# Kernel optimization log

Hardware: AMD Instinct MI355X
Metric: run time of the kernel (lower is better)

The kernel has to match this reference:

```python
import jax, jax.numpy as jnp
import numpy as np

B, T, H = 4, 2048, 1024
NH = 16
HD = H // NH  # 64
FF = 4 * H


def setup_inputs() -> dict:
    key = jax.random.key(0)
    ks = jax.random.split(key, 11)
    s = 0.02
    return {
        "x": jax.random.normal(ks[0], (B, T, H), dtype=jnp.float32),
        "Wq": jax.random.normal(ks[1], (H, H), dtype=jnp.float32) * s,
        "bq": jnp.zeros((H,), dtype=jnp.float32),
        "Wk": jax.random.normal(ks[2], (H, H), dtype=jnp.float32) * s,
        "bk": jnp.zeros((H,), dtype=jnp.float32),
        "Wv": jax.random.normal(ks[3], (H, H), dtype=jnp.float32) * s,
        "bv": jnp.zeros((H,), dtype=jnp.float32),
        "W1": jax.random.normal(ks[4], (H, FF), dtype=jnp.float32) * s,
        "b1": jnp.zeros((FF,), dtype=jnp.float32),
        "W2": jax.random.normal(ks[5], (FF, H), dtype=jnp.float32) * s,
        "b2": jnp.zeros((H,), dtype=jnp.float32),
    }


def _block(x, Wq, bq, Wk, bk, Wv, bv, W1, b1, W2, b2):
    b, t, h = x.shape
    # multi-head masked self-attention; NOTE: scale = full h_dim ** 0.5 (as in source)
    q = (x @ Wq + bq).reshape(b, t, NH, HD).transpose(0, 2, 1, 3)  # [B,nH,T,HD]
    k = (x @ Wk + bk).reshape(b, t, NH, HD).transpose(0, 2, 1, 3)
    v = (x @ Wv + bv).reshape(b, t, NH, HD).transpose(0, 2, 1, 3)
    att = jnp.einsum("bnqd,bnkd->bnqk", q, k) / (h ** 0.5)  # [B,nH,T,T]
    causal = jnp.tril(jnp.ones((t, t), dtype=bool))
    att = jnp.where(causal, att, -jnp.inf)
    w = jax.nn.softmax(att, axis=-1)
    attn_out = jnp.einsum("bnqk,bnkd->bnqd", w, v).transpose(0, 2, 1, 3).reshape(b, t, h)
    x = x + attn_out
    # MLP (dropout p=0 -> identity)
    mlp = jax.nn.gelu(x @ W1 + b1) @ W2 + b2
    return x + mlp


def reference(x, Wq, bq, Wk, bk, Wv, bv, W1, b1, W2, b2):
    return _block(x, Wq, bq, Wk, bk, Wv, bv, W1, b1, W2, b2)
```

## Files before the change

### kernel.cpp

```cpp
#include <hip/hip_runtime.h>
#include <cstdint>
#include <cstddef>

typedef unsigned short u16;
typedef __attribute__((ext_vector_type(8))) __bf16 bf16x8;
typedef __attribute__((ext_vector_type(4))) __bf16 bf16x4;
typedef __attribute__((ext_vector_type(4))) float f32x4;
typedef __attribute__((ext_vector_type(4))) u16 u16x4;

#define MFMA(a, b, c) __builtin_amdgcn_mfma_f32_16x16x32_bf16((a), (b), (c), 0, 0, 0)

__device__ __forceinline__ u16 f2b(float f) {
  union { __bf16 h; u16 u; } v;
  v.h = (__bf16)f;
  return v.u;
}

__device__ __forceinline__ void gld16(const void* g, void* l) {
  __builtin_amdgcn_global_load_lds(
      (__attribute__((address_space(1))) void*)(void*)(g),
      (__attribute__((address_space(3))) void*)(l), 16, 0, 0);
}

__device__ __forceinline__ size_t qk_off(int t, int hd) {
  return (size_t)((((t >> 4) * 2 + (hd >> 5)) * 512)
                  + ((((hd >> 3) & 3) * 16 + (t & 15)) * 8) + (hd & 7));
}
__device__ __forceinline__ size_t v_off(int t, int hd) {
  int kk = ((t & 15) << 2) | ((t >> 4) & 3);
  return (size_t)(((t >> 6) * 4096)
                  + (((hd >> 4) * 2 + (kk >> 5)) * 512)
                  + ((((kk >> 3) & 3) * 16 + (hd & 15)) * 8) + (kk & 7));
}

__global__ void xconv(const float* __restrict__ in, u16* __restrict__ out, int n) {
  int i = (blockIdx.x * blockDim.x + threadIdx.x) * 4;
  if (i >= n) return;
  float4 v = *(const float4*)(in + i);
  u16x4 o;
  o[0] = f2b(v.x); o[1] = f2b(v.y); o[2] = f2b(v.z); o[3] = f2b(v.w);
  *(u16x4*)(out + i) = o;
}

__global__ void wtrans_all(const float* __restrict__ Wq, const float* __restrict__ Wk,
                           const float* __restrict__ Wv, const float* __restrict__ W1,
                           const float* __restrict__ W2, u16* __restrict__ Wqkvt,
                           u16* __restrict__ W1t, u16* __restrict__ W2t) {
  __shared__ float tile[32][33];
  int blk = blockIdx.x;
  const float* W;
  u16* Wt;
  int Kd, Nd, nx;
  if (blk < 3072) {
    int s = blk >> 10;
    blk &= 1023;
    W = (s == 0) ? Wq : (s == 1) ? Wk : Wv;
    Wt = Wqkvt + (size_t)s * 1048576;
    Kd = 1024; Nd = 1024; nx = 32;
  } else if (blk < 7168) {
    blk -= 3072; W = W1; Wt = W1t; Kd = 1024; Nd = 4096; nx = 128;
  } else {
    blk -= 7168; W = W2; Wt = W2t; Kd = 4096; Nd = 1024; nx = 32;
  }
  int n0 = (blk % nx) * 32, k0 = (blk / nx) * 32;
  int tx = threadIdx.x, ty = threadIdx.y;
#pragma unroll
  for (int i = 0; i < 4; i++)
    tile[ty + i * 8][tx] = W[(size_t)(k0 + ty + i * 8) * Nd + n0 + tx];
  __syncthreads();
#pragma unroll
  for (int i = 0; i < 4; i++)
    Wt[(size_t)(n0 + ty + i * 8) * Kd + k0 + tx] = f2b(tile[tx][ty + i * 8]);
}

template <int MODE>
__global__ __launch_bounds__(512, 2) void gemm8p(
    const u16* __restrict__ A, const u16* __restrict__ Bt,
    const float* __restrict__ b0, void* __restrict__ outp,
    int N, int K) {
  __shared__ __attribute__((aligned(16))) u16 As_[2][16384];
  __shared__ __attribute__((aligned(16))) u16 Bs_[2][16384];
  const int tid = threadIdx.x;
  const int wid = tid >> 6, lane = tid & 63;
  const int g = lane >> 4, r = lane & 15;

  const int xcd = blockIdx.x & 7;
  const int ii = blockIdx.x >> 3;
  const int c4 = ii >> 4, w = ii & 15;
  const int bm = xcd * 4 + (w >> 2);
  const int bn = c4 * 4 + (w & 3);

  const int mrow = (wid >> 2) * 64;
  const int ncol = (wid & 3) * 32;

  const int ko0 = ((0 * 4 + g) ^ (r & 7)) * 8;
  const int ko1 = ((1 * 4 + g) ^ (r & 7)) * 8;

  size_t aOff[4], bOff[4];
#pragma unroll
  for (int i4 = 0; i4 < 4; i4++) {
    int cc = i4 * 512 + tid, row = cc >> 3;
    int js = ((cc & 7) ^ (row & 7)) * 8;
    aOff[i4] = (size_t)(bm * 256 + row) * K + js;
    bOff[i4] = (size_t)(bn * 256 + row) * K + js;
  }

  f32x4 acc[8][4];
  const f32x4 zero4 = {0.f, 0.f, 0.f, 0.f};
#pragma unroll
  for (int i = 0; i < 8; i++)
#pragma unroll
    for (int j = 0; j < 4; j++) acc[i][j] = zero4;

#pragma unroll
  for (int i4 = 0; i4 < 4; i4++) {
    gld16(A + aOff[i4], &As_[0][(i4 * 512 + tid) * 8]);
    gld16(Bt + bOff[i4], &Bs_[0][(i4 * 512 + tid) * 8]);
  }
  gld16(A + aOff[0] + 64, &As_[1][(0 * 512 + tid) * 8]);
  gld16(A + aOff[1] + 64, &As_[1][(1 * 512 + tid) * 8]);
  gld16(Bt + bOff[2] + 64, &Bs_[1][(2 * 512 + tid) * 8]);
  gld16(Bt + bOff[3] + 64, &Bs_[1][(3 * 512 + tid) * 8]);
  asm volatile("s_waitcnt vmcnt(4)" ::: "memory");
  __builtin_amdgcn_s_barrier();

  const int KT = K >> 6;
  for (int t = 0; t < KT; ++t) {
    const int p = t & 1, pn = p ^ 1;
    const u16* as = As_[p];
    const u16* bs = Bs_[p];
    const bool m1 = (t + 1) < KT, m2 = (t + 2) < KT;
    const size_t k1 = (size_t)(t + 1) * 64, k2 = (size_t)(t + 2) * 64;
    bf16x8 af[4][2], bf[2][2];

#pragma unroll
    for (int mt = 0; mt < 4; mt++) {
      int rw = mrow + mt * 16 + r;
      af[mt][0] = *(const bf16x8*)&as[rw * 64 + ko0];
      af[mt][1] = *(const bf16x8*)&as[rw * 64 + ko1];
    }
#pragma unroll
    for (int nt = 0; nt < 2; nt++) {
      int rw = ncol + nt * 16 + r;
      bf[nt][0] = *(const bf16x8*)&bs[rw * 64 + ko0];
      bf[nt][1] = *(const bf16x8*)&bs[rw * 64 + ko1];
    }
    if (m1) {
      gld16(A + aOff[2] + k1, &As_[pn][(1024 + tid) * 8]);
      gld16(A + aOff[3] + k1, &As_[pn][(1536 + tid) * 8]);
    }
    __builtin_amdgcn_s_barrier();
    asm volatile("s_waitcnt lgkmcnt(0)" ::: "memory");
    __builtin_amdgcn_sched_barrier(0);
    __builtin_amdgcn_s_setprio(1);
#pragma unroll
    for (int mt = 0; mt < 4; mt++)
#pragma unroll
      for (int nt = 0; nt < 2; nt++)
        acc[mt][nt] = MFMA(af[mt][1], bf[nt][1], MFMA(af[mt][0], bf[nt][0], acc[mt][nt]));
    __builtin_amdgcn_s_setprio(0);
    __builtin_amdgcn_s_barrier();

#pragma unroll
    for (int nt = 0; nt < 2; nt++) {
      int rw = 128 + ncol + nt * 16 + r;
      bf[nt][0] = *(const bf16x8*)&bs[rw * 64 + ko0];
      bf[nt][1] = *(const bf16x8*)&bs[rw * 64 + ko1];
    }
    if (m1) {
      gld16(Bt + bOff[0] + k1, &Bs_[pn][(tid) * 8]);
      gld16(Bt + bOff[1] + k1, &Bs_[pn][(512 + tid) * 8]);
    }
    __builtin_amdgcn_s_barrier();
    asm volatile("s_waitcnt lgkmcnt(0)" ::: "memory");
    __builtin_amdgcn_sched_barrier(0);
    __builtin_amdgcn_s_setprio(1);
#pragma unroll
    for (int mt = 0; mt < 4; mt++)
#pragma unroll
      for (int nt = 0; nt < 2; nt++)
        acc[mt][2 + nt] = MFMA(af[mt][1], bf[nt][1], MFMA(af[mt][0], bf[nt][0], acc[mt][2 + nt]));
    __builtin_amdgcn_s_setprio(0);
    __builtin_amdgcn_s_barrier();

#pragma unroll
    for (int mt = 0; mt < 4; mt++) {
      int rw = 128 + mrow + mt * 16 + r;
      af[mt][0] = *(const bf16x8*)&as[rw * 64 + ko0];
      af[mt][1] = *(const bf16x8*)&as[rw * 64 + ko1];
    }
    if (m2) {
      gld16(A + aOff[0] + k2, &As_[p][(tid) * 8]);
      gld16(A + aOff[1] + k2, &As_[p][(512 + tid) * 8]);
    }
    __builtin_amdgcn_s_barrier();
    asm volatile("s_waitcnt lgkmcnt(0)" ::: "memory");
    __builtin_amdgcn_sched_barrier(0);
    __builtin_amdgcn_s_setprio(1);
#pragma unroll
    for (int mt = 0; mt < 4; mt++)
#pragma unroll
      for (int nt = 0; nt < 2; nt++)
        acc[4 + mt][2 + nt] = MFMA(af[mt][1], bf[nt][1], MFMA(af[mt][0], bf[nt][0], acc[4 + mt][2 + nt]));
    __builtin_amdgcn_s_setprio(0);
    __builtin_amdgcn_s_barrier();

#pragma unroll
    for (int nt = 0; nt < 2; nt++) {
      int rw = ncol + nt * 16 + r;
      bf[nt][0] = *(const bf16x8*)&bs[rw * 64 + ko0];
      bf[nt][1] = *(const bf16x8*)&bs[rw * 64 + ko1];
    }
    if (m2) {
      gld16(Bt + bOff[2] + k2, &Bs_[p][(1024 + tid) * 8]);
      gld16(Bt + bOff[3] + k2, &Bs_[p][(1536 + tid) * 8]);
    }
    __builtin_amdgcn_s_barrier();
    asm volatile("s_waitcnt lgkmcnt(0)" ::: "memory");
    __builtin_amdgcn_sched_barrier(0);
    __builtin_amdgcn_s_setprio(1);
#pragma unroll
    for (int mt = 0; mt < 4; mt++)
#pragma unroll
      for (int nt = 0; nt < 2; nt++)
        acc[4 + mt][nt] = MFMA(af[mt][1], bf[nt][1], MFMA(af[mt][0], bf[nt][0], acc[4 + mt][nt]));
    __builtin_amdgcn_s_setprio(0);
    if (m2) asm volatile("s_waitcnt vmcnt(4)" ::: "memory");
    else    asm volatile("s_waitcnt vmcnt(0)" ::: "memory");
    __builtin_amdgcn_s_barrier();
  }

#pragma unroll
  for (int am = 0; am < 8; am++) {
#pragma unroll
    for (int an = 0; an < 4; an++) {
      int col = bn * 256 + (an >> 1) * 128 + ncol + (an & 1) * 16 + r;
      float bv = b0[col];
#pragma unroll
      for (int q = 0; q < 4; q++) {
        int row = bm * 256 + (am >> 2) * 128 + mrow + (am & 3) * 16 + g * 4 + q;
        float v = acc[am][an][q] + bv;
        if (MODE == 2) {
          const float c1 = -2.3025850929940457f;
          const float c2 = c1 * 0.044715f;
          float t2 = v * v;
          float z = v * (c1 + c2 * t2);
          float sg = 1.0f / (1.0f + __builtin_amdgcn_exp2f(z));
          ((u16*)outp)[(size_t)row * N + col] = f2b(v * sg);
        }
      }
    }
  }
}

template <int MODE>
__global__ __launch_bounds__(512, 2) void gemm256(
    const u16* __restrict__ A, const u16* __restrict__ Bt,
    const float* __restrict__ b0, const float* __restrict__ b1,
    const float* __restrict__ b2, void* __restrict__ outp,
    const float* __restrict__ resid, int N, int K, float scale) {
  __shared__ __attribute__((aligned(16))) u16 As_[3][16384];
  __shared__ __attribute__((aligned(16))) u16 Bs_[3][8192];
  const int tid = threadIdx.x;
  const int wid = tid >> 6, lane = tid & 63;
  const int g = lane >> 4, r = lane & 15;

  const int xcd = blockIdx.x & 7;
  const int ii = blockIdx.x >> 3;
  const int bm = xcd * 4 + ((ii & 31) >> 3);
  const int bn = (ii >> 5) * 8 + (ii & 7);

  const int wrow = (wid >> 1) * 64;
  const int wcol = (wid & 1) * 64;

  const int ko0 = ((0 * 4 + g) ^ (r & 7)) * 8;
  const int ko1 = ((1 * 4 + g) ^ (r & 7)) * 8;

  size_t aOff[4], bOff[2];
#pragma unroll
  for (int i4 = 0; i4 < 4; i4++) {
    int cc = i4 * 512 + tid, row = cc >> 3;
    int js = ((cc & 7) ^ (row & 7)) * 8;
    aOff[i4] = (size_t)(bm * 256 + row) * K + js;
  }
#pragma unroll
  for (int i2 = 0; i2 < 2; i2++) {
    int cc = i2 * 512 + tid, row = cc >> 3;
    int js = ((cc & 7) ^ (row & 7)) * 8;
    bOff[i2] = (size_t)(bn * 128 + row) * K + js;
  }

  f32x4 acc[4][4];
  const f32x4 zero4 = {0.f, 0.f, 0.f, 0.f};
#pragma unroll
  for (int i = 0; i < 4; i++)
#pragma unroll
    for (int j = 0; j < 4; j++) acc[i][j] = zero4;

#pragma unroll
  for (int i4 = 0; i4 < 4; i4++) gld16(A + aOff[i4], &As_[0][(i4 * 512 + tid) * 8]);
#pragma unroll
  for (int i2 = 0; i2 < 2; i2++) gld16(Bt + bOff[i2], &Bs_[0][(i2 * 512 + tid) * 8]);
#pragma unroll
  for (int i4 = 0; i4 < 4; i4++) gld16(A + aOff[i4] + 64, &As_[1][(i4 * 512 + tid) * 8]);
#pragma unroll
  for (int i2 = 0; i2 < 2; i2++) gld16(Bt + bOff[i2] + 64, &Bs_[1][(i2 * 512 + tid) * 8]);
  asm volatile("s_waitcnt vmcnt(6)" ::: "memory");
  __builtin_amdgcn_s_barrier();

  const int KT = K >> 6;
  int cur = 0;
  for (int t = 0; t < KT; ++t) {
    const u16* as = As_[cur];
    const u16* bs = Bs_[cur];
    const int stg = (cur == 0) ? 2 : cur - 1;
    const bool more = (t + 2) < KT;
    const size_t k2 = (size_t)(t + 2) * 64;

    bf16x8 af0[4], bf0[4], af1[4], bf1[4];
#pragma unroll
    for (int mt = 0; mt < 4; mt++) {
      af0[mt] = *(const bf16x8*)&as[(wrow + mt * 16 + r) * 64 + ko0];
      af1[mt] = *(const bf16x8*)&as[(wrow + mt * 16 + r) * 64 + ko1];
    }
#pragma unroll
    for (int nt = 0; nt < 4; nt++) {
      bf0[nt] = *(const bf16x8*)&bs[(wcol + nt * 16 + r) * 64 + ko0];
      bf1[nt] = *(const bf16x8*)&bs[(wcol + nt * 16 + r) * 64 + ko1];
    }

    if (more) {
#pragma unroll
      for (int i4 = 0; i4 < 4; i4++)
        gld16(A + aOff[i4] + k2, &As_[stg][(i4 * 512 + tid) * 8]);
#pragma unroll
      for (int i2 = 0; i2 < 2; i2++)
        gld16(Bt + bOff[i2] + k2, &Bs_[stg][(i2 * 512 + tid) * 8]);
    }

#pragma unroll
    for (int mt = 0; mt < 4; mt++)
#pragma unroll
      for (int nt = 0; nt < 4; nt++)
        acc[mt][nt] = MFMA(af0[mt], bf0[nt], acc[mt][nt]);
#pragma unroll
    for (int mt = 0; mt < 4; mt++)
#pragma unroll
      for (int nt = 0; nt < 4; nt++)
        acc[mt][nt] = MFMA(af1[mt], bf1[nt], acc[mt][nt]);

    if (t + 1 < KT) {
      if (more) asm volatile("s_waitcnt vmcnt(6)" ::: "memory");
      else      asm volatile("s_waitcnt vmcnt(0)" ::: "memory");
    }
    __builtin_amdgcn_s_barrier();
    cur = (cur == 2) ? 0 : cur + 1;
  }

#pragma unroll
  for (int mt = 0; mt < 4; mt++) {
#pragma unroll
    for (int nt = 0; nt < 4; nt++) {
      int col = bn * 128 + wcol + nt * 16 + r;
      float bv;
      if (MODE == 4) {
        int sec = col >> 10, hcol = col & 1023;
        bv = (sec == 0) ? b0[hcol] : (sec == 1) ? b1[hcol] : b2[hcol];
      } else {
        bv = b0[col];
      }
#pragma unroll
      for (int q = 0; q < 4; q++) {
        int row = bm * 256 + wrow + mt * 16 + g * 4 + q;
        float v = acc[mt][nt][q] + bv;
        if (MODE == 3) {
          ((float*)outp)[(size_t)row * N + col] = v + resid[(size_t)row * N + col];
        } else if (MODE == 4) {
          int sec = col >> 10, hcol = col & 1023;
          int head = hcol >> 6, hd = hcol & 63;
          int bb = row >> 11, tt = row & 2047;
          size_t hbase = ((size_t)bb * 16 + head) * 131072;
          u16* qout = (u16*)outp;
          if (sec == 0) {
            qout[hbase + qk_off(tt, hd)] = f2b(v * scale);
          } else if (sec == 1) {
            (qout + 8388608)[hbase + qk_off(tt, hd)] = f2b(v);
          } else {
            (qout + 16777216)[hbase + v_off(tt, hd)] = f2b(v);
          }
        }
      }
    }
  }
}

__global__ __launch_bounds__(256) void attn_kernel(
    const u16* __restrict__ Q, const u16* __restrict__ Kc,
    const u16* __restrict__ Vt, const float* __restrict__ x,
    float* __restrict__ x1, u16* __restrict__ xb1) {
  const int bh = blockIdx.x & 63;
  const int slot = blockIdx.x >> 6;
  const int tid = threadIdx.x;
  const int wid = tid >> 6, lane = tid & 63;
  const int g = lane >> 4, c = lane & 15;
  const u16* Qh = Q + (size_t)bh * 131072;
  const u16* Kh = Kc + (size_t)bh * 131072;
  const u16* Vh = Vt + (size_t)bh * 131072;
  const int b = bh >> 4, head = bh & 15;

  __shared__ __attribute__((aligned(16))) u16 Ks[8192];
  __shared__ __attribute__((aligned(16))) u16 Vs[8192];
  __shared__ __attribute__((aligned(16))) u16 P[4][32][72];

  bf16x8 ones;
#pragma unroll
  for (int i = 0; i < 8; i++) ones[i] = (__bf16)1.0f;

  const f32x4 zero4 = {0.f, 0.f, 0.f, 0.f};

  for (int phase = 0; phase < 2; ++phase) {
    const int bt = phase ? (15 - slot) : slot;
    const int q0b = bt * 128;
    const int q0 = q0b + wid * 32;
    const int kendw = q0 + 32;
    const int nkt = bt + 1;

    bf16x8 qf[2][2];
#pragma unroll
    for (int mt = 0; mt < 2; mt++)
#pragma unroll
      for (int h = 0; h < 2; h++)
        qf[mt][h] = *(const bf16x8*)&Qh[(((q0 >> 4) + mt) * 2 + h) * 512 + lane * 8];

    f32x4 o[2][4];
    f32x4 lac[2];
#pragma unroll
    for (int mt = 0; mt < 2; mt++) {
      lac[mt] = zero4;
#pragma unroll
      for (int i = 0; i < 4; i++) o[mt][i] = zero4;
    }

    for (int kt = 0; kt < nkt; ++kt) {
      const int k0 = kt * 128;
#pragma unroll
      for (int r2 = 0; r2 < 4; r2++) {
        int idx = (r2 * 256 + tid) * 8;
        gld16(Kh + (size_t)k0 * 64 + idx, Ks + idx);
        gld16(Vh + (size_t)k0 * 64 + idx, Vs + idx);
      }
      __syncthreads();

#pragma unroll
      for (int s2 = 0; s2 < 2; ++s2) {
        const int k0s = k0 + s2 * 64;
        if (k0s < kendw) {
          bf16x8 kf[4][2], vf[4][2];
#pragma unroll
          for (int nt = 0; nt < 4; nt++)
#pragma unroll
            for (int h = 0; h < 2; h++) {
              kf[nt][h] = *(const bf16x8*)&Ks[s2 * 4096 + (nt * 2 + h) * 512 + lane * 8];
              vf[nt][h] = *(const bf16x8*)&Vs[s2 * 4096 + (nt * 2 + h) * 512 + lane * 8];
            }

          f32x4 sv[2][4];
#pragma unroll
          for (int mt = 0; mt < 2; mt++)
#pragma unroll
            for (int nt = 0; nt < 4; nt++) sv[mt][nt] = zero4;
#pragma unroll
          for (int nt = 0; nt < 4; nt++)
#pragma unroll
            for (int mt = 0; mt < 2; mt++) {
              sv[mt][nt] = MFMA(qf[mt][0], kf[nt][0], sv[mt][nt]);
              sv[mt][nt] = MFMA(qf[mt][1], kf[nt][1], sv[mt][nt]);
            }

          if (k0s + 64 > q0) {
#pragma unroll
            for (int mt = 0; mt < 2; mt++)
#pragma unroll
              for (int rr = 0; rr < 4; rr++) {
                int q = q0 + mt * 16 + g * 4 + rr;
#pragma unroll
                for (int nt = 0; nt < 4; nt++)
                  if (k0s + nt * 16 + c > q) sv[mt][nt][rr] = -1e30f;
              }
          }

#pragma unroll
          for (int mt = 0; mt < 2; mt++)
#pragma unroll
            for (int rr = 0; rr < 4; rr++) {
              union { u16x4 u; bf16x4 h; } pw;
#pragma unroll
              for (int nt = 0; nt < 4; nt++)
                pw.h[nt] = (__bf16)__builtin_amdgcn_exp2f(sv[mt][nt][rr]);
              *(u16x4*)&P[wid][mt * 16 + g * 4 + rr][4 * c] = pw.u;
            }

          asm volatile("s_waitcnt lgkmcnt(0)" ::: "memory");

#pragma unroll
          for (int mt = 0; mt < 2; mt++) {
            bf16x8 pf0 = *(const bf16x8*)&P[wid][mt * 16 + c][g * 8];
            bf16x8 pf1 = *(const bf16x8*)&P[wid][mt * 16 + c][32 + g * 8];
            lac[mt] = MFMA(pf0, ones, lac[mt]);
            lac[mt] = MFMA(pf1, ones, lac[mt]);
#pragma unroll
            for (int ot = 0; ot < 4; ot++) {
              f32x4 oo = MFMA(pf0, vf[ot][0], o[mt][ot]);
              o[mt][ot] = MFMA(pf1, vf[ot][1], oo);
            }
          }
        }
      }
      __syncthreads();
    }

    float inv[2][4];
#pragma unroll
    for (int mt = 0; mt < 2; mt++)
#pragma unroll
      for (int rr = 0; rr < 4; rr++) inv[mt][rr] = 1.0f / lac[mt][rr];
#pragma unroll
    for (int mt = 0; mt < 2; mt++)
#pragma unroll
      for (int ot = 0; ot < 4; ot++)
#pragma unroll
        for (int rr = 0; rr < 4; rr++) {
          int t = q0 + mt * 16 + g * 4 + rr;
          int hd = ot * 16 + c;
          size_t xi = ((size_t)b * 2048 + t) * 1024 + head * 64 + hd;
          float v = x[xi] + o[mt][ot][rr] * inv[mt][rr];
          x1[xi] = v;
          xb1[xi] = f2b(v);
        }
  }
}

extern "C" void kernel_launch(void* const* d_in, const int* in_sizes, int n_in,
                              void* d_out, int out_size, void* d_ws, size_t ws_size,
                              hipStream_t stream) {
  (void)in_sizes; (void)n_in; (void)out_size; (void)ws_size;
  const float* x = (const float*)d_in[0];
  const float* Wq = (const float*)d_in[1];
  const float* bq = (const float*)d_in[2];
  const float* Wk = (const float*)d_in[3];
  const float* bk = (const float*)d_in[4];
  const float* Wv = (const float*)d_in[5];
  const float* bv = (const float*)d_in[6];
  const float* W1 = (const float*)d_in[7];
  const float* b1 = (const float*)d_in[8];
  const float* W2 = (const float*)d_in[9];
  const float* b2 = (const float*)d_in[10];

  char* ws = (char*)d_ws;
  size_t off = 0;
  auto alloc = [&](size_t bytes) {
    char* p = ws + off;
    off += (bytes + 255) & ~(size_t)255;
    return p;
  };
  u16* xb    = (u16*)alloc(8192ull * 1024 * 2);
  u16* Wqkvt = (u16*)alloc(3072ull * 1024 * 2);
  u16* W1t   = (u16*)alloc(4096ull * 1024 * 2);
  u16* W2t   = (u16*)alloc(1024ull * 4096 * 2);
  u16* Qb    = (u16*)alloc(3ull * 8192 * 1024 * 2);
  float* x1  = (float*)alloc(8192ull * 1024 * 4);
  u16* hb    = (u16*)alloc(8192ull * 4096 * 2);
  u16* xb1   = xb;
  u16* Kb    = Qb + 8388608;
  u16* Vtb   = Qb + 16777216;

  const float qscale = 1.4426950408889634f / 32.0f;

  xconv<<<dim3(8192), dim3(256), 0, stream>>>(x, xb, 8192 * 1024);
  wtrans_all<<<dim3(11264), dim3(32, 8), 0, stream>>>(
      Wq, Wk, Wv, W1, W2, Wqkvt, W1t, W2t);
  gemm256<4><<<dim3(768), dim3(512), 0, stream>>>(
      xb, Wqkvt, bq, bk, bv, Qb, nullptr, 3072, 1024, qscale);
  attn_kernel<<<dim3(512), dim3(256), 0, stream>>>(Qb, Kb, Vtb, x, x1, xb1);
  gemm8p<2><<<dim3(512), dim3(512), 0, stream>>>(
      xb1, W1t, b1, hb, 4096, 1024);
  gemm256<3><<<dim3(256), dim3(512), 0, stream>>>(
      hb, W2t, b2, nullptr, nullptr, d_out, x1, 1024, 4096, 1.0f);
}
```

Before: 425.5 us.

## Make W1 GEMM persistent over two N tiles and merge prep kernels

The FC1 GEMM now launches 256 blocks, and each block computes two 256-wide N tiles in sequence. It issues the first global-to-LDS loads for the second tile before running the GELU epilogue of the first, so that epilogue overlaps the next tile's prologue and the tail wave is removed. The x conversion and weight transpose kernels are also merged into one launch to save a kernel launch. The risk is that the grid now covers only one block per CU slot at 2 blocks/CU, which may lower the latency hiding that came from co-resident blocks.

```diff
diff --git a/kernel.cpp b/kernel.cpp
--- a/kernel.cpp
+++ b/kernel.cpp
@@ -33,21 +33,23 @@
                   + ((((kk >> 3) & 3) * 16 + (hd & 15)) * 8) + (kk & 7));
 }
 
-__global__ void xconv(const float* __restrict__ in, u16* __restrict__ out, int n) {
-  int i = (blockIdx.x * blockDim.x + threadIdx.x) * 4;
-  if (i >= n) return;
-  float4 v = *(const float4*)(in + i);
-  u16x4 o;
-  o[0] = f2b(v.x); o[1] = f2b(v.y); o[2] = f2b(v.z); o[3] = f2b(v.w);
-  *(u16x4*)(out + i) = o;
-}
-
-__global__ void wtrans_all(const float* __restrict__ Wq, const float* __restrict__ Wk,
-                           const float* __restrict__ Wv, const float* __restrict__ W1,
-                           const float* __restrict__ W2, u16* __restrict__ Wqkvt,
-                           u16* __restrict__ W1t, u16* __restrict__ W2t) {
+__global__ void prep(const float* __restrict__ x, u16* __restrict__ xb,
+                     const float* __restrict__ Wq, const float* __restrict__ Wk,
+                     const float* __restrict__ Wv, const float* __restrict__ W1,
+                     const float* __restrict__ W2, u16* __restrict__ Wqkvt,
+                     u16* __restrict__ W1t, u16* __restrict__ W2t) {
+  int blk = blockIdx.x;
+  int tx = threadIdx.x, ty = threadIdx.y;
+  if (blk < 8192) {
+    int i = (blk * 256 + ty * 32 + tx) * 4;
+    float4 v = *(const float4*)(x + i);
+    u16x4 o;
+    o[0] = f2b(v.x); o[1] = f2b(v.y); o[2] = f2b(v.z); o[3] = f2b(v.w);
+    *(u16x4*)(xb + i) = o;
+    return;
+  }
+  blk -= 8192;
   __shared__ float tile[32][33];
-  int blk = blockIdx.x;
   const float* W;
   u16* Wt;
   int Kd, Nd, nx;
@@ -63,7 +65,6 @@
     blk -= 7168; W = W2; Wt = W2t; Kd = 4096; Nd = 1024; nx = 32;
   }
   int n0 = (blk % nx) * 32, k0 = (blk / nx) * 32;
-  int tx = threadIdx.x, ty = threadIdx.y;
 #pragma unroll
   for (int i = 0; i < 4; i++)
     tile[ty + i * 8][tx] = W[(size_t)(k0 + ty + i * 8) * Nd + n0 + tx];
@@ -86,9 +87,8 @@
 
   const int xcd = blockIdx.x & 7;
   const int ii = blockIdx.x >> 3;
-  const int c4 = ii >> 4, w = ii & 15;
-  const int bm = xcd * 4 + (w >> 2);
-  const int bn = c4 * 4 + (w & 3);
+  const int bm = xcd * 4 + (ii >> 3);
+  const int bnp = ii & 7;
 
   const int mrow = (wid >> 2) * 64;
   const int ncol = (wid & 3) * 32;
@@ -96,157 +96,186 @@
   const int ko0 = ((0 * 4 + g) ^ (r & 7)) * 8;
   const int ko1 = ((1 * 4 + g) ^ (r & 7)) * 8;
 
-  size_t aOff[4], bOff[4];
+  size_t aOff[4];
+  int arow_[4], js_[4];
 #pragma unroll
   for (int i4 = 0; i4 < 4; i4++) {
     int cc = i4 * 512 + tid, row = cc >> 3;
     int js = ((cc & 7) ^ (row & 7)) * 8;
+    arow_[i4] = row; js_[i4] = js;
     aOff[i4] = (size_t)(bm * 256 + row) * K + js;
-    bOff[i4] = (size_t)(bn * 256 + row) * K + js;
-  }
-
-  f32x4 acc[8][4];
-  const f32x4 zero4 = {0.f, 0.f, 0.f, 0.f};
-#pragma unroll
-  for (int i = 0; i < 8; i++)
-#pragma unroll
-    for (int j = 0; j < 4; j++) acc[i][j] = zero4;
-
-#pragma unroll
-  for (int i4 = 0; i4 < 4; i4++) {
-    gld16(A + aOff[i4], &As_[0][(i4 * 512 + tid) * 8]);
-    gld16(Bt + bOff[i4], &Bs_[0][(i4 * 512 + tid) * 8]);
-  }
-  gld16(A + aOff[0] + 64, &As_[1][(0 * 512 + tid) * 8]);
-  gld16(A + aOff[1] + 64, &As_[1][(1 * 512 + tid) * 8]);
-  gld16(Bt + bOff[2] + 64, &Bs_[1][(2 * 512 + tid) * 8]);
-  gld16(Bt + bOff[3] + 64, &Bs_[1][(3 * 512 + tid) * 8]);
-  asm volatile("s_waitcnt vmcnt(4)" ::: "memory");
-  __builtin_amdgcn_s_barrier();
+  }
 
   const int KT = K >> 6;
-  for (int t = 0; t < KT; ++t) {
-    const int p = t & 1, pn = p ^ 1;
-    const u16* as = As_[p];
-    const u16* bs = Bs_[p];
-    const bool m1 = (t + 1) < KT, m2 = (t + 2) < KT;
-    const size_t k1 = (size_t)(t + 1) * 64, k2 = (size_t)(t + 2) * 64;
-    bf16x8 af[4][2], bf[2][2];
-
-#pragma unroll
-    for (int mt = 0; mt < 4; mt++) {
-      int rw = mrow + mt * 16 + r;
-      af[mt][0] = *(const bf16x8*)&as[rw * 64 + ko0];
-      af[mt][1] = *(const bf16x8*)&as[rw * 64 + ko1];
-    }
-#pragma unroll
-    for (int nt = 0; nt < 2; nt++) {
-      int rw = ncol + nt * 16 + r;
-      bf[nt][0] = *(const bf16x8*)&bs[rw * 64 + ko0];
-      bf[nt][1] = *(const bf16x8*)&bs[rw * 64 + ko1];
-    }
-    if (m1) {
-      gld16(A + aOff[2] + k1, &As_[pn][(1024 + tid) * 8]);
-      gld16(A + aOff[3] + k1, &As_[pn][(1536 + tid) * 8]);
-    }
+
+  for (int rep = 0; rep < 2; ++rep) {
+    const int bn = bnp + rep * 8;
+    size_t bOff[4];
+#pragma unroll
+    for (int i4 = 0; i4 < 4; i4++)
+      bOff[i4] = (size_t)(bn * 256 + arow_[i4]) * K + js_[i4];
+
+    f32x4 acc[8][4];
+    const f32x4 zero4 = {0.f, 0.f, 0.f, 0.f};
+#pragma unroll
+    for (int i = 0; i < 8; i++)
+#pragma unroll
+      for (int j = 0; j < 4; j++) acc[i][j] = zero4;
+
+    if (rep == 0) {
+#pragma unroll
+      for (int i4 = 0; i4 < 4; i4++) {
+        gld16(A + aOff[i4], &As_[0][(i4 * 512 + tid) * 8]);
+        gld16(Bt + bOff[i4], &Bs_[0][(i4 * 512 + tid) * 8]);
+      }
+      gld16(A + aOff[0] + 64, &As_[1][(0 * 512 + tid) * 8]);
+      gld16(A + aOff[1] + 64, &As_[1][(1 * 512 + tid) * 8]);
+      gld16(Bt + bOff[2] + 64, &Bs_[1][(2 * 512 + tid) * 8]);
+      gld16(Bt + bOff[3] + 64, &Bs_[1][(3 * 512 + tid) * 8]);
+    }
+    asm volatile("s_waitcnt vmcnt(4)" ::: "memory");
     __builtin_amdgcn_s_barrier();
-    asm volatile("s_waitcnt lgkmcnt(0)" ::: "memory");
-    __builtin_amdgcn_sched_barrier(0);
-    __builtin_amdgcn_s_setprio(1);
-#pragma unroll
-    for (int mt = 0; mt < 4; mt++)
-#pragma unroll
-      for (int nt = 0; nt < 2; nt++)
-        acc[mt][nt] = MFMA(af[mt][1], bf[nt][1], MFMA(af[mt][0], bf[nt][0], acc[mt][nt]));
-    __builtin_amdgcn_s_setprio(0);
-    __builtin_amdgcn_s_barrier();
-
-#pragma unroll
-    for (int nt = 0; nt < 2; nt++) {
-      int rw = 128 + ncol + nt * 16 + r;
-      bf[nt][0] = *(const bf16x8*)&bs[rw * 64 + ko0];
-      bf[nt][1] = *(const bf16x8*)&bs[rw * 64 + ko1];
-    }
-    if (m1) {
-      gld16(Bt + bOff[0] + k1, &Bs_[pn][(tid) * 8]);
-      gld16(Bt + bOff[1] + k1, &Bs_[pn][(512 + tid) * 8]);
-    }
-    __builtin_amdgcn_s_barrier();
-    asm volatile("s_waitcnt lgkmcnt(0)" ::: "memory");
-    __builtin_amdgcn_sched_barrier(0);
-    __builtin_amdgcn_s_setprio(1);
-#pragma unroll
-    for (int mt = 0; mt < 4; mt++)
-#pragma unroll
-      for (int nt = 0; nt < 2; nt++)
-        acc[mt][2 + nt] = MFMA(af[mt][1], bf[nt][1], MFMA(af[mt][0], bf[nt][0], acc[mt][2 + nt]));
-    __builtin_amdgcn_s_setprio(0);
-    __builtin_amdgcn_s_barrier();
-
-#pragma unroll
-    for (int mt = 0; mt < 4; mt++) {
-      int rw = 128 + mrow + mt * 16 + r;
-      af[mt][0] = *(const bf16x8*)&as[rw * 64 + ko0];
-      af[mt][1] = *(const bf16x8*)&as[rw * 64 + ko1];
-    }
-    if (m2) {
-      gld16(A + aOff[0] + k2, &As_[p][(tid) * 8]);
-      gld16(A + aOff[1] + k2, &As_[p][(512 + tid) * 8]);
-    }
-    __builtin_amdgcn_s_barrier();
-    asm volatile("s_waitcnt lgkmcnt(0)" ::: "memory");
-    __builtin_amdgcn_sched_barrier(0);
-    __builtin_amdgcn_s_setprio(1);
-#pragma unroll
-    for (int mt = 0; mt < 4; mt++)
-#pragma unroll
-      for (int nt = 0; nt < 2; nt++)
-        acc[4 + mt][2 + nt] = MFMA(af[mt][1], bf[nt][1], MFMA(af[mt][0], bf[nt][0], acc[4 + mt][2 + nt]));
-    __builtin_amdgcn_s_setprio(0);
-    __builtin_amdgcn_s_barrier();
-
-#pragma unroll
-    for (int nt = 0; nt < 2; nt++) {
-      int rw = ncol + nt * 16 + r;
-      bf[nt][0] = *(const bf16x8*)&bs[rw * 64 + ko0];
-      bf[nt][1] = *(const bf16x8*)&bs[rw * 64 + ko1];
-    }
-    if (m2) {
-      gld16(Bt + bOff[2] + k2, &Bs_[p][(1024 + tid) * 8]);
-      gld16(Bt + bOff[3] + k2, &Bs_[p][(1536 + tid) * 8]);
-    }
-    __builtin_amdgcn_s_barrier();
-    asm volatile("s_waitcnt lgkmcnt(0)" ::: "memory");
-    __builtin_amdgcn_sched_barrier(0);
-    __builtin_amdgcn_s_setprio(1);
-#pragma unroll
-    for (int mt = 0; mt < 4; mt++)
-#pragma unroll
-      for (int nt = 0; nt < 2; nt++)
-        acc[4 + mt][nt] = MFMA(af[mt][1], bf[nt][1], MFMA(af[mt][0], bf[nt][0], acc[4 + mt][nt]));
-    __builtin_amdgcn_s_setprio(0);
-    if (m2) asm volatile("s_waitcnt vmcnt(4)" ::: "memory");
-    else    asm volatile("s_waitcnt vmcnt(0)" ::: "memory");
-    __builtin_amdgcn_s_barrier();
-  }
-
-#pragma unroll
-  for (int am = 0; am < 8; am++) {
-#pragma unroll
-    for (int an = 0; an < 4; an++) {
-      int col = bn * 256 + (an >> 1) * 128 + ncol + (an & 1) * 16 + r;
-      float bv = b0[col];
-#pragma unroll
-      for (int q = 0; q < 4; q++) {
-        int row = bm * 256 + (am >> 2) * 128 + mrow + (am & 3) * 16 + g * 4 + q;
-        float v = acc[am][an][q] + bv;
-        if (MODE == 2) {
-          const float c1 = -2.3025850929940457f;
-          const float c2 = c1 * 0.044715f;
-          float t2 = v * v;
-          float z = v * (c1 + c2 * t2);
-          float sg = 1.0f / (1.0f + __builtin_amdgcn_exp2f(z));
-          ((u16*)outp)[(size_t)row * N + col] = f2b(v * sg);
+
+    for (int t = 0; t < KT; ++t) {
+      const int p = t & 1, pn = p ^ 1;
+      const u16* as = As_[p];
+      const u16* bs = Bs_[p];
+      const bool m1 = (t + 1) < KT, m2 = (t + 2) < KT;
+      const size_t k1 = (size_t)(t + 1) * 64, k2 = (size_t)(t + 2) * 64;
+      bf16x8 af[4][2], bf[2][2];
+
+#pragma unroll
+      for (int mt = 0; mt < 4; mt++) {
+        int rw = mrow + mt * 16 + r;
+        af[mt][0] = *(const bf16x8*)&as[rw * 64 + ko0];
+        af[mt][1] = *(const bf16x8*)&as[rw * 64 + ko1];
+      }
+#pragma unroll
+      for (int nt = 0; nt < 2; nt++) {
+        int rw = ncol + nt * 16 + r;
+        bf[nt][0] = *(const bf16x8*)&bs[rw * 64 + ko0];
+        bf[nt][1] = *(const bf16x8*)&bs[rw * 64 + ko1];
+      }
+      if (m1) {
+        gld16(A + aOff[2] + k1, &As_[pn][(1024 + tid) * 8]);
+        gld16(A + aOff[3] + k1, &As_[pn][(1536 + tid) * 8]);
+      }
+      __builtin_amdgcn_s_barrier();
+      asm volatile("s_waitcnt lgkmcnt(0)" ::: "memory");
+      __builtin_amdgcn_sched_barrier(0);
+      __builtin_amdgcn_s_setprio(1);
+#pragma unroll
+      for (int mt = 0; mt < 4; mt++)
+#pragma unroll
+        for (int nt = 0; nt < 2; nt++)
+          acc[mt][nt] = MFMA(af[mt][1], bf[nt][1], MFMA(af[mt][0], bf[nt][0], acc[mt][nt]));
+      __builtin_amdgcn_s_setprio(0);
+      __builtin_amdgcn_s_barrier();
+
+#pragma unroll
+      for (int nt = 0; nt < 2; nt++) {
+        int rw = 128 + ncol + nt * 16 + r;
+        bf[nt][0] = *(const bf16x8*)&bs[rw * 64 + ko0];
+        bf[nt][1] = *(const bf16x8*)&bs[rw * 64 + ko1];
+      }
+      if (m1) {
+        gld16(Bt + bOff[0] + k1, &Bs_[pn][(tid) * 8]);
+        gld16(Bt + bOff[1] + k1, &Bs_[pn][(512 + tid) * 8]);
+      }
+      __builtin_amdgcn_s_barrier();
+      asm volatile("s_waitcnt lgkmcnt(0)" ::: "memory");
+      __builtin_amdgcn_sched_barrier(0);
+      __builtin_amdgcn_s_setprio(1);
+#pragma unroll
+      for (int mt = 0; mt < 4; mt++)
+#pragma unroll
+        for (int nt = 0; nt < 2; nt++)
+          acc[mt][2 + nt] = MFMA(af[mt][1], bf[nt][1], MFMA(af[mt][0], bf[nt][0], acc[mt][2 + nt]));
+      __builtin_amdgcn_s_setprio(0);
+      __builtin_amdgcn_s_barrier();
+
+#pragma unroll
+      for (int mt = 0; mt < 4; mt++) {
+        int rw = 128 + mrow + mt * 16 + r;
+        af[mt][0] = *(const bf16x8*)&as[rw * 64 + ko0];
+        af[mt][1] = *(const bf16x8*)&as[rw * 64 + ko1];
+      }
+      if (m2) {
+        gld16(A + aOff[0] + k2, &As_[p][(tid) * 8]);
+        gld16(A + aOff[1] + k2, &As_[p][(512 + tid) * 8]);
+      }
+      __builtin_amdgcn_s_barrier();
+      asm volatile("s_waitcnt lgkmcnt(0)" ::: "memory");
+      __builtin_amdgcn_sched_barrier(0);
+      __builtin_amdgcn_s_setprio(1);
+#pragma unroll
+      for (int mt = 0; mt < 4; mt++)
+#pragma unroll
+        for (int nt = 0; nt < 2; nt++)
+          acc[4 + mt][2 + nt] = MFMA(af[mt][1], bf[nt][1], MFMA(af[mt][0], bf[nt][0], acc[4 + mt][2 + nt]));
+      __builtin_amdgcn_s_setprio(0);
+      __builtin_amdgcn_s_barrier();
+
+#pragma unroll
+      for (int nt = 0; nt < 2; nt++) {
+        int rw = ncol + nt * 16 + r;
+        bf[nt][0] = *(const bf16x8*)&bs[rw * 64 + ko0];
+        bf[nt][1] = *(const bf16x8*)&bs[rw * 64 + ko1];
+      }
+      if (m2) {
+        gld16(Bt + bOff[2] + k2, &Bs_[p][(1024 + tid) * 8]);
+        gld16(Bt + bOff[3] + k2, &Bs_[p][(1536 + tid) * 8]);
+      }
+      __builtin_amdgcn_s_barrier();
+      asm volatile("s_waitcnt lgkmcnt(0)" ::: "memory");
+      __builtin_amdgcn_sched_barrier(0);
+      __builtin_amdgcn_s_setprio(1);
+#pragma unroll
+      for (int mt = 0; mt < 4; mt++)
+#pragma unroll
+        for (int nt = 0; nt < 2; nt++)
+          acc[4 + mt][nt] = MFMA(af[mt][1], bf[nt][1], MFMA(af[mt][0], bf[nt][0], acc[4 + mt][nt]));
+      __builtin_amdgcn_s_setprio(0);
+      if (m2) asm volatile("s_waitcnt vmcnt(4)" ::: "memory");
+      else    asm volatile("s_waitcnt vmcnt(0)" ::: "memory");
+      __builtin_amdgcn_s_barrier();
+    }
+
+    if (rep == 0) {
+      const int bn1 = bnp + 8;
+      size_t bOff1;
+#pragma unroll
+      for (int i4 = 0; i4 < 4; i4++) {
+        bOff1 = (size_t)(bn1 * 256 + arow_[i4]) * K + js_[i4];
+        gld16(A + aOff[i4], &As_[0][(i4 * 512 + tid) * 8]);
+        gld16(Bt + bOff1, &Bs_[0][(i4 * 512 + tid) * 8]);
+      }
+      gld16(A + aOff[0] + 64, &As_[1][(0 * 512 + tid) * 8]);
+      gld16(A + aOff[1] + 64, &As_[1][(1 * 512 + tid) * 8]);
+      gld16(Bt + (size_t)(bn1 * 256 + arow_[2]) * K + js_[2] + 64,
+            &Bs_[1][(2 * 512 + tid) * 8]);
+      gld16(Bt + (size_t)(bn1 * 256 + arow_[3]) * K + js_[3] + 64,
+            &Bs_[1][(3 * 512 + tid) * 8]);
+    }
+
+#pragma unroll
+    for (int am = 0; am < 8; am++) {
+#pragma unroll
+      for (int an = 0; an < 4; an++) {
+        int col = bn * 256 + (an >> 1) * 128 + ncol + (an & 1) * 16 + r;
+        float bv = b0[col];
+#pragma unroll
+        for (int q = 0; q < 4; q++) {
+          int row = bm * 256 + (am >> 2) * 128 + mrow + (am & 3) * 16 + g * 4 + q;
+          float v = acc[am][an][q] + bv;
+          if (MODE == 2) {
+            const float c1 = -2.3025850929940457f;
+            const float c2 = c1 * 0.044715f;
+            float t2 = v * v;
+            float z = v * (c1 + c2 * t2);
+            float sg = 1.0f / (1.0f + __builtin_amdgcn_exp2f(z));
+            ((u16*)outp)[(size_t)row * N + col] = f2b(v * sg);
+          }
         }
       }
     }
@@ -576,13 +605,12 @@
 
   const float qscale = 1.4426950408889634f / 32.0f;
 
-  xconv<<<dim3(8192), dim3(256), 0, stream>>>(x, xb, 8192 * 1024);
-  wtrans_all<<<dim3(11264), dim3(32, 8), 0, stream>>>(
-      Wq, Wk, Wv, W1, W2, Wqkvt, W1t, W2t);
+  prep<<<dim3(19456), dim3(32, 8), 0, stream>>>(
+      x, xb, Wq, Wk, Wv, W1, W2, Wqkvt, W1t, W2t);
   gemm256<4><<<dim3(768), dim3(512), 0, stream>>>(
       xb, Wqkvt, bq, bk, bv, Qb, nullptr, 3072, 1024, qscale);
   attn_kernel<<<dim3(512), dim3(256), 0, stream>>>(Qb, Kb, Vtb, x, x1, xb1);
-  gemm8p<2><<<dim3(512), dim3(512), 0, stream>>>(
+  gemm8p<2><<<dim3(256), dim3(512), 0, stream>>>(
       xb1, W1t, b1, hb, 4096, 1024);
   gemm256<3><<<dim3(256), dim3(512), 0, stream>>>(
       hb, W2t, b2, nullptr, nullptr, d_out, x1, 1024, 4096, 1.0f);
```

Result: slower. 450.4 us (+5.8%).

## Prefetch next K/V tile during second half-tile compute; merge prep kernels

Applied to the files above, without the earlier changes.

The attention loop now issues the global-to-LDS loads for the next 128-key K/V tile right after the second 64-key half has been pulled into registers, so those loads overlap with that half's MFMA and softmax work instead of stalling at the top of each iteration. The first tile is loaded before the loop. Separately, the x-to-bf16 conversion and the weight transpose kernels are merged into one launch to save a kernel launch. The cost is more registers held for the second half's K/V fragments, which could lower occupancy.

```diff
diff --git a/kernel.cpp b/kernel.cpp
--- a/kernel.cpp
+++ b/kernel.cpp
@@ -33,21 +33,23 @@
                   + ((((kk >> 3) & 3) * 16 + (hd & 15)) * 8) + (kk & 7));
 }
 
-__global__ void xconv(const float* __restrict__ in, u16* __restrict__ out, int n) {
-  int i = (blockIdx.x * blockDim.x + threadIdx.x) * 4;
-  if (i >= n) return;
-  float4 v = *(const float4*)(in + i);
-  u16x4 o;
-  o[0] = f2b(v.x); o[1] = f2b(v.y); o[2] = f2b(v.z); o[3] = f2b(v.w);
-  *(u16x4*)(out + i) = o;
-}
-
-__global__ void wtrans_all(const float* __restrict__ Wq, const float* __restrict__ Wk,
-                           const float* __restrict__ Wv, const float* __restrict__ W1,
-                           const float* __restrict__ W2, u16* __restrict__ Wqkvt,
-                           u16* __restrict__ W1t, u16* __restrict__ W2t) {
+__global__ void prep(const float* __restrict__ x, u16* __restrict__ xb,
+                     const float* __restrict__ Wq, const float* __restrict__ Wk,
+                     const float* __restrict__ Wv, const float* __restrict__ W1,
+                     const float* __restrict__ W2, u16* __restrict__ Wqkvt,
+                     u16* __restrict__ W1t, u16* __restrict__ W2t) {
+  int blk = blockIdx.x;
+  int tx = threadIdx.x, ty = threadIdx.y;
+  if (blk < 8192) {
+    int i = (blk * 256 + ty * 32 + tx) * 4;
+    float4 v = *(const float4*)(x + i);
+    u16x4 o;
+    o[0] = f2b(v.x); o[1] = f2b(v.y); o[2] = f2b(v.z); o[3] = f2b(v.w);
+    *(u16x4*)(xb + i) = o;
+    return;
+  }
+  blk -= 8192;
   __shared__ float tile[32][33];
-  int blk = blockIdx.x;
   const float* W;
   u16* Wt;
   int Kd, Nd, nx;
@@ -63,7 +65,6 @@
     blk -= 7168; W = W2; Wt = W2t; Kd = 4096; Nd = 1024; nx = 32;
   }
   int n0 = (blk % nx) * 32, k0 = (blk / nx) * 32;
-  int tx = threadIdx.x, ty = threadIdx.y;
 #pragma unroll
   for (int i = 0; i < 4; i++)
     tile[ty + i * 8][tx] = W[(size_t)(k0 + ty + i * 8) * Nd + n0 + tx];
@@ -420,8 +421,7 @@
 
   for (int phase = 0; phase < 2; ++phase) {
     const int bt = phase ? (15 - slot) : slot;
-    const int q0b = bt * 128;
-    const int q0 = q0b + wid * 32;
+    const int q0 = bt * 128 + wid * 32;
     const int kendw = q0 + 32;
     const int nkt = bt + 1;
 
@@ -441,82 +441,155 @@
       for (int i = 0; i < 4; i++) o[mt][i] = zero4;
     }
 
+#pragma unroll
+    for (int r2 = 0; r2 < 4; r2++) {
+      int idx = (r2 * 256 + tid) * 8;
+      gld16(Kh + idx, Ks + idx);
+      gld16(Vh + idx, Vs + idx);
+    }
+
     for (int kt = 0; kt < nkt; ++kt) {
       const int k0 = kt * 128;
-#pragma unroll
-      for (int r2 = 0; r2 < 4; r2++) {
-        int idx = (r2 * 256 + tid) * 8;
-        gld16(Kh + (size_t)k0 * 64 + idx, Ks + idx);
-        gld16(Vh + (size_t)k0 * 64 + idx, Vs + idx);
+      __syncthreads();
+
+      {
+        bf16x8 kf[4][2], vf[4][2];
+#pragma unroll
+        for (int nt = 0; nt < 4; nt++)
+#pragma unroll
+          for (int h = 0; h < 2; h++) {
+            kf[nt][h] = *(const bf16x8*)&Ks[(nt * 2 + h) * 512 + lane * 8];
+            vf[nt][h] = *(const bf16x8*)&Vs[(nt * 2 + h) * 512 + lane * 8];
+          }
+
+        f32x4 sv[2][4];
+#pragma unroll
+        for (int mt = 0; mt < 2; mt++)
+#pragma unroll
+          for (int nt = 0; nt < 4; nt++) sv[mt][nt] = zero4;
+#pragma unroll
+        for (int nt = 0; nt < 4; nt++)
+#pragma unroll
+          for (int mt = 0; mt < 2; mt++) {
+            sv[mt][nt] = MFMA(qf[mt][0], kf[nt][0], sv[mt][nt]);
+            sv[mt][nt] = MFMA(qf[mt][1], kf[nt][1], sv[mt][nt]);
+          }
+
+        if (k0 + 64 > q0) {
+#pragma unroll
+          for (int mt = 0; mt < 2; mt++)
+#pragma unroll
+            for (int rr = 0; rr < 4; rr++) {
+              int q = q0 + mt * 16 + g * 4 + rr;
+#pragma unroll
+              for (int nt = 0; nt < 4; nt++)
+                if (k0 + nt * 16 + c > q) sv[mt][nt][rr] = -1e30f;
+            }
+        }
+
+#pragma unroll
+        for (int mt = 0; mt < 2; mt++)
+#pragma unroll
+          for (int rr = 0; rr < 4; rr++) {
+            union { u16x4 u; bf16x4 h; } pw;
+#pragma unroll
+            for (int nt = 0; nt < 4; nt++)
+              pw.h[nt] = (__bf16)__builtin_amdgcn_exp2f(sv[mt][nt][rr]);
+            *(u16x4*)&P[wid][mt * 16 + g * 4 + rr][4 * c] = pw.u;
+          }
+
+        asm volatile("s_waitcnt lgkmcnt(0)" ::: "memory");
+
+#pragma unroll
+        for (int mt = 0; mt < 2; mt++) {
+          bf16x8 pf0 = *(const bf16x8*)&P[wid][mt * 16 + c][g * 8];
+          bf16x8 pf1 = *(const bf16x8*)&P[wid][mt * 16 + c][32 + g * 8];
+          lac[mt] = MFMA(pf0, ones, lac[mt]);
+          lac[mt] = MFMA(pf1, ones, lac[mt]);
+#pragma unroll
+          for (int ot = 0; ot < 4; ot++) {
+            f32x4 oo = MFMA(pf0, vf[ot][0], o[mt][ot]);
+            o[mt][ot] = MFMA(pf1, vf[ot][1], oo);
+          }
+        }
+      }
+
+      const int k0s1 = k0 + 64;
+      const bool do1 = (k0s1 < kendw);
+      bf16x8 kf1[4][2], vf1[4][2];
+      if (do1) {
+#pragma unroll
+        for (int nt = 0; nt < 4; nt++)
+#pragma unroll
+          for (int h = 0; h < 2; h++) {
+            kf1[nt][h] = *(const bf16x8*)&Ks[4096 + (nt * 2 + h) * 512 + lane * 8];
+            vf1[nt][h] = *(const bf16x8*)&Vs[4096 + (nt * 2 + h) * 512 + lane * 8];
+          }
       }
       __syncthreads();
 
-#pragma unroll
-      for (int s2 = 0; s2 < 2; ++s2) {
-        const int k0s = k0 + s2 * 64;
-        if (k0s < kendw) {
-          bf16x8 kf[4][2], vf[4][2];
-#pragma unroll
-          for (int nt = 0; nt < 4; nt++)
-#pragma unroll
-            for (int h = 0; h < 2; h++) {
-              kf[nt][h] = *(const bf16x8*)&Ks[s2 * 4096 + (nt * 2 + h) * 512 + lane * 8];
-              vf[nt][h] = *(const bf16x8*)&Vs[s2 * 4096 + (nt * 2 + h) * 512 + lane * 8];
+      if (kt + 1 < nkt) {
+        const size_t kb = (size_t)(kt + 1) * 128 * 64;
+#pragma unroll
+        for (int r2 = 0; r2 < 4; r2++) {
+          int idx = (r2 * 256 + tid) * 8;
+          gld16(Kh + kb + idx, Ks + idx);
+          gld16(Vh + kb + idx, Vs + idx);
+        }
+      }
+
+      if (do1) {
+        f32x4 sv[2][4];
+#pragma unroll
+        for (int mt = 0; mt < 2; mt++)
+#pragma unroll
+          for (int nt = 0; nt < 4; nt++) sv[mt][nt] = zero4;
+#pragma unroll
+        for (int nt = 0; nt < 4; nt++)
+#pragma unroll
+          for (int mt = 0; mt < 2; mt++) {
+            sv[mt][nt] = MFMA(qf[mt][0], kf1[nt][0], sv[mt][nt]);
+            sv[mt][nt] = MFMA(qf[mt][1], kf1[nt][1], sv[mt][nt]);
+          }
+
+        if (k0s1 + 64 > q0) {
+#pragma unroll
+          for (int mt = 0; mt < 2; mt++)
+#pragma unroll
+            for (int rr = 0; rr < 4; rr++) {
+              int q = q0 + mt * 16 + g * 4 + rr;
+#pragma unroll
+              for (int nt = 0; nt < 4; nt++)
+                if (k0s1 + nt * 16 + c > q) sv[mt][nt][rr] = -1e30f;
             }
-
-          f32x4 sv[2][4];
-#pragma unroll
-          for (int mt = 0; mt < 2; mt++)
-#pragma unroll
-            for (int nt = 0; nt < 4; nt++) sv[mt][nt] = zero4;
-#pragma unroll
-          for (int nt = 0; nt < 4; nt++)
-#pragma unroll
-            for (int mt = 0; mt < 2; mt++) {
-              sv[mt][nt] = MFMA(qf[mt][0], kf[nt][0], sv[mt][nt]);
-              sv[mt][nt] = MFMA(qf[mt][1], kf[nt][1], sv[mt][nt]);
-            }
-
-          if (k0s + 64 > q0) {
-#pragma unroll
-            for (int mt = 0; mt < 2; mt++)
-#pragma unroll
-              for (int rr = 0; rr < 4; rr++) {
-                int q = q0 + mt * 16 + g * 4 + rr;
-#pragma unroll
-                for (int nt = 0; nt < 4; nt++)
-                  if (k0s + nt * 16 + c > q) sv[mt][nt][rr] = -1e30f;
-              }
-          }
-
-#pragma unroll
-          for (int mt = 0; mt < 2; mt++)
-#pragma unroll
-            for (int rr = 0; rr < 4; rr++) {
-              union { u16x4 u; bf16x4 h; } pw;
-#pragma unroll
-              for (int nt = 0; nt < 4; nt++)
-                pw.h[nt] = (__bf16)__builtin_amdgcn_exp2f(sv[mt][nt][rr]);
-              *(u16x4*)&P[wid][mt * 16 + g * 4 + rr][4 * c] = pw.u;
-            }
-
-          asm volatile("s_waitcnt lgkmcnt(0)" ::: "memory");
-
-#pragma unroll
-          for (int mt = 0; mt < 2; mt++) {
-            bf16x8 pf0 = *(const bf16x8*)&P[wid][mt * 16 + c][g * 8];
-            bf16x8 pf1 = *(const bf16x8*)&P[wid][mt * 16 + c][32 + g * 8];
-            lac[mt] = MFMA(pf0, ones, lac[mt]);
-            lac[mt] = MFMA(pf1, ones, lac[mt]);
-#pragma unroll
-            for (int ot = 0; ot < 4; ot++) {
-              f32x4 oo = MFMA(pf0, vf[ot][0], o[mt][ot]);
-              o[mt][ot] = MFMA(pf1, vf[ot][1], oo);
-            }
+        }
+
+#pragma unroll
+        for (int mt = 0; mt < 2; mt++)
+#pragma unroll
+          for (int rr = 0; rr < 4; rr++) {
+            union { u16x4 u; bf16x4 h; } pw;
+#pragma unroll
+            for (int nt = 0; nt < 4; nt++)
+              pw.h[nt] = (__bf16)__builtin_amdgcn_exp2f(sv[mt][nt][rr]);
+            *(u16x4*)&P[wid][mt * 16 + g * 4 + rr][4 * c] = pw.u;
+          }
+
+        asm volatile("s_waitcnt lgkmcnt(0)" ::: "memory");
+
+#pragma unroll
+        for (int mt = 0; mt < 2; mt++) {
+          bf16x8 pf0 = *(const bf16x8*)&P[wid][mt * 16 + c][g * 8];
+          bf16x8 pf1 = *(const bf16x8*)&P[wid][mt * 16 + c][32 + g * 8];
+          lac[mt] = MFMA(pf0, ones, lac[mt]);
+          lac[mt] = MFMA(pf1, ones, lac[mt]);
+#pragma unroll
+          for (int ot = 0; ot < 4; ot++) {
+            f32x4 oo = MFMA(pf0, vf1[ot][0], o[mt][ot]);
+            o[mt][ot] = MFMA(pf1, vf1[ot][1], oo);
           }
         }
       }
-      __syncthreads();
     }
 
     float inv[2][4];
@@ -576,9 +649,8 @@
 
   const float qscale = 1.4426950408889634f / 32.0f;
 
-  xconv<<<dim3(8192), dim3(256), 0, stream>>>(x, xb, 8192 * 1024);
-  wtrans_all<<<dim3(11264), dim3(32, 8), 0, stream>>>(
-      Wq, Wk, Wv, W1, W2, Wqkvt, W1t, W2t);
+  prep<<<dim3(19456), dim3(32, 8), 0, stream>>>(
+      x, xb, Wq, Wk, Wv, W1, W2, Wqkvt, W1t, W2t);
   gemm256<4><<<dim3(768), dim3(512), 0, stream>>>(
       xb, Wqkvt, bq, bk, bv, Qb, nullptr, 3072, 1024, qscale);
   attn_kernel<<<dim3(512), dim3(256), 0, stream>>>(Qb, Kb, Vtb, x, x1, xb1);
```

Measured after the change: 435.4 us. +2.3%, slower.
